# Kernel tuning notes

Measured on AMD Instinct MI355X. Metric: run time of the kernel, lower is better.

The kernel has to match this reference:

```python
import jax, jax.numpy as jnp
import numpy as np

B, V, K, D, E, NE = 32, 512, 16, 128, 32, 8192


def setup_inputs() -> dict:
    key = jax.random.key(0)
    ks = jax.random.split(key, 12)
    s = 0.05
    return {
        "vertex_features": jax.random.normal(ks[0], (B, V, D), jnp.float32),
        "atom_adj": jax.random.randint(ks[1], (B * V * K,), 0, B * V),
        "bond_adj": jax.random.randint(ks[2], (B * V * K,), 0, B * NE),
        "h0": jax.random.normal(ks[3], (B, V, D), jnp.float32),
        "lamda": jnp.full((1,), 0.5, jnp.float32),
        "alpha": jnp.full((1,), 0.1, jnp.float32),
        "l": 1,
        "edge_initial": jax.random.normal(ks[4], (B, NE, E), jnp.float32),
        "vertex_mask": jnp.ones((B, V), jnp.float32),
        "nbs_mask": jax.random.uniform(ks[5], (B, V, K), jnp.float32),
        # label_U1: (D+E) -> D ; label_U2: 2D -> D ; feature_updating: D -> D (variant=False)
        "W1": jax.random.normal(ks[6], (D, D + E), jnp.float32) * s,
        "b1": jax.random.normal(ks[7], (D,), jnp.float32) * s,
        "W2": jax.random.normal(ks[8], (D, 2 * D), jnp.float32) * s,
        "b2": jax.random.normal(ks[9], (D,), jnp.float32) * s,
        "W3": jax.random.normal(ks[10], (D, D), jnp.float32) * s,
        "b3": jax.random.normal(ks[11], (D,), jnp.float32) * s,
    }


def reference(vertex_features, atom_adj, bond_adj, h0, lamda, alpha, l,
              edge_initial, vertex_mask, nbs_mask, W1, b1, W2, b2, W3, b3):
    b, v = vertex_mask.shape
    k = nbs_mask.shape[2]
    d = vertex_features.shape[-1]
    e = edge_initial.shape[-1]
    # gather neighbor vertex and edge features (flat index, torch.index_select semantics)
    vn = vertex_features.reshape(-1, d)[atom_adj].reshape(b, v, k, d)
    en = edge_initial.reshape(-1, e)[bond_adj].reshape(b, v, k, e)
    l_neighbor = jnp.concatenate([vn, en], axis=-1)            # [b,v,k,d+e]
    nl = jax.nn.gelu(l_neighbor @ W1.T + b1, approximate=False)  # exact GELU like torch F.gelu
    nl = jnp.sum(nl * nbs_mask[..., None], axis=-2)            # masked sum over neighbors -> [b,v,d]
    hi = jnp.concatenate([nl, vertex_features], axis=-1) @ W2.T + b2
    theta = jnp.log(lamda / l + 1.0)                           # broadcast scalar (shape [1])
    support = (1.0 - alpha) * hi + alpha * h0                  # variant=False: r == support
    out = theta * (support @ W3.T + b3) + (1.0 - theta) * support
    out = out + vertex_features                                # residual=True
    return out
```

## Files before the change

kernel.cpp:

```cpp
#include <hip/hip_runtime.h>
#include <hip/hip_bf16.h>
#include <math.h>

#define NLSTR 136
#define ASTR  168

typedef __bf16 bf16x8 __attribute__((ext_vector_type(8)));
typedef float f32x4 __attribute__((ext_vector_type(4)));
typedef float f32x16 __attribute__((ext_vector_type(16)));
typedef unsigned short ushort8v __attribute__((ext_vector_type(8)));

union FragU { ushort8v u; bf16x8 b; };

static __device__ inline unsigned short f2bf(float f){
  unsigned u = __float_as_uint(f);
  u += 0x7fffu + ((u >> 16) & 1u);
  return (unsigned short)(u >> 16);
}
static __device__ inline float bf2f(unsigned short u){
  return __uint_as_float(((unsigned)u) << 16);
}
static __device__ inline unsigned pk2(float a, float b){
  union { __hip_bfloat162 h; unsigned u; } r;
  r.h = __float22bfloat162_rn(float2{a, b});
  return r.u;
}
static __device__ inline ushort8v pkcvt8(float4 a, float4 b){
  union { unsigned u[4]; ushort8v v; } r;
  r.u[0] = pk2(a.x, a.y); r.u[1] = pk2(a.z, a.w);
  r.u[2] = pk2(b.x, b.y); r.u[3] = pk2(b.z, b.w);
  return r.v;
}

static __device__ inline float gelu_f(float x){
  float u = x * x;
  float p = fmaf(u, -0.1029434273f, -2.3022084765f);
  float e = __builtin_amdgcn_exp2f(x * p);
  return x * __builtin_amdgcn_rcpf(1.0f + e);
}

#define WG_BARRIER() asm volatile("s_waitcnt lgkmcnt(0)\n\ts_barrier" ::: "memory")

__global__ __launch_bounds__(256) void prep_kernel(
    const float* __restrict__ vf, const float* __restrict__ W1,
    const float* __restrict__ W2, const float* __restrict__ W3,
    unsigned short* __restrict__ vfbf, unsigned short* __restrict__ w1f,
    unsigned short* __restrict__ w2f, unsigned short* __restrict__ w3f)
{
  int t = blockIdx.x * 256 + threadIdx.x;
  if (t < 262144){
    const float4* src = (const float4*)vf;
    float4 x = src[t * 2], y = src[t * 2 + 1];
    *(ushort8v*)(vfbf + t * 8) = pkcvt8(x, y);
    return;
  }
  int t2 = t - 262144;
  const float* s;
  unsigned short* d;
  if (t2 < 2560){
    int fragid = t2 >> 6, lane = t2 & 63;
    int nc2 = fragid / 10, kc = fragid % 10, n = lane & 31, h = lane >> 5;
    s = W1 + (nc2 * 32 + n) * 160 + kc * 16 + h * 8;
    d = w1f + t2 * 8;
  } else if (t2 < 6656){
    int t3 = t2 - 2560;
    int fragid = t3 >> 6, lane = t3 & 63;
    int kc = fragid >> 3, nc = fragid & 7, col = lane & 15, quad = lane >> 4;
    s = W2 + (nc * 16 + col) * 256 + kc * 32 + quad * 8;
    d = w2f + t3 * 8;
  } else if (t2 < 8704){
    int t3 = t2 - 6656;
    int fragid = t3 >> 6, lane = t3 & 63;
    int kc = fragid >> 3, nc = fragid & 7, col = lane & 15, quad = lane >> 4;
    s = W3 + (nc * 16 + col) * 128 + kc * 32 + quad * 8;
    d = w3f + t3 * 8;
  } else return;
#pragma unroll
  for (int j = 0; j < 8; j++) d[j] = f2bf(s[j]);
}

__global__ __launch_bounds__(256, 4) void fused_kernel(
    const unsigned short* __restrict__ vfbf,
    const float* __restrict__ vf,
    const int* __restrict__ aadj, const int* __restrict__ badj,
    const float* __restrict__ edge, const float* __restrict__ nbs,
    const float* __restrict__ h0,
    const unsigned short* __restrict__ w1f, const unsigned short* __restrict__ w2f,
    const unsigned short* __restrict__ w3f,
    const float* __restrict__ b1, const float* __restrict__ b2, const float* __restrict__ b3,
    const float* __restrict__ lamda, const float* __restrict__ alpha,
    const int* __restrict__ lval,
    float* __restrict__ out)
{
  __shared__ __align__(16) unsigned short abuf[2][32 * ASTR];
  __shared__ __align__(16) unsigned short nl_lds[16 * NLSTR];
  __shared__ __align__(16) unsigned short sup_lds[16 * NLSTR];
  __shared__ __align__(16) float nbs_lds[256];
  const int wid  = threadIdx.x >> 6;
  const int lane = threadIdx.x & 63;
  const int n32  = lane & 31;
  const int h    = lane >> 5;
  const int col  = lane & 15;
  const int quad = lane >> 4;
  const int v0   = blockIdx.x * 16;

  const int srow = threadIdx.x >> 3;
  const int ssub = threadIdx.x & 7;

  nbs_lds[threadIdx.x] = nbs[v0 * 16 + threadIdx.x];

  int a_all[8], e_all[8];
  {
    const int base = (v0 + (srow >> 4)) * 16 + (srow & 15);
#pragma unroll
    for (int p = 0; p < 8; p++){
      a_all[p] = aadj[base + 32 * p];
      e_all[p] = badj[base + 32 * p];
    }
  }

  ushort8v sv[3][2]; float4 se[3];
#pragma unroll
  for (int s = 0; s < 3; s++){
    const ushort8v* vs = (const ushort8v*)(vfbf + (size_t)a_all[s] * 128 + ssub * 16);
    sv[s][0] = vs[0]; sv[s][1] = vs[1];
    se[s] = *(const float4*)(edge + (size_t)e_all[s] * 32 + ssub * 4);
  }

  FragU bw[10];
#pragma unroll
  for (int kc = 0; kc < 10; kc++)
    bw[kc].u = *(const ushort8v*)(w1f + ((wid * 10 + kc) * 64 + lane) * 8);

  const float bb1 = b1[wid * 32 + n32];

  {
    unsigned short* dst = abuf[0] + srow * ASTR + ssub * 16;
    *(ushort8v*)dst = sv[0][0]; *(ushort8v*)(dst + 8) = sv[0][1];
    unsigned* ed = (unsigned*)(abuf[0] + srow * ASTR + 128 + ssub * 4);
    ed[0] = pk2(se[0].x, se[0].y); ed[1] = pk2(se[0].z, se[0].w);
  }

  const float4* nbsl = (const float4*)nbs_lds;

#pragma unroll
  for (int p = 0; p < 8; ++p){
    WG_BARRIER();

    if (p < 7){
      const int s = (p + 1) % 3;
      unsigned short* dst = abuf[(p + 1) & 1] + srow * ASTR + ssub * 16;
      *(ushort8v*)dst = sv[s][0]; *(ushort8v*)(dst + 8) = sv[s][1];
      unsigned* ed = (unsigned*)(abuf[(p + 1) & 1] + srow * ASTR + 128 + ssub * 4);
      ed[0] = pk2(se[s].x, se[s].y); ed[1] = pk2(se[s].z, se[s].w);
    }
    if (p < 5){
      const int s = (p + 3) % 3;
      const ushort8v* vs = (const ushort8v*)(vfbf + (size_t)a_all[p + 3] * 128 + ssub * 16);
      sv[s][0] = vs[0]; sv[s][1] = vs[1];
      se[s] = *(const float4*)(edge + (size_t)e_all[p + 3] * 32 + ssub * 4);
    }

    const float4 mAlo = nbsl[8 * p + h],     mAhi = nbsl[8 * p + 2 + h];
    const float4 mBlo = nbsl[8 * p + 4 + h], mBhi = nbsl[8 * p + 6 + h];

    const unsigned short* ab = abuf[p & 1] + n32 * ASTR + h * 8;
    f32x16 acc = {};
#pragma unroll
    for (int kc = 0; kc < 10; kc++){
      FragU fa;
      fa.u = *(const ushort8v*)(ab + kc * 16);
      acc = __builtin_amdgcn_mfma_f32_32x32x16_bf16(fa.b, bw[kc].b, acc, 0, 0, 0);
    }

    {
      float sA = gelu_f(acc[0] + bb1) * mAlo.x + gelu_f(acc[1] + bb1) * mAlo.y
               + gelu_f(acc[2] + bb1) * mAlo.z + gelu_f(acc[3] + bb1) * mAlo.w
               + gelu_f(acc[4] + bb1) * mAhi.x + gelu_f(acc[5] + bb1) * mAhi.y
               + gelu_f(acc[6] + bb1) * mAhi.z + gelu_f(acc[7] + bb1) * mAhi.w;
      float sB = gelu_f(acc[8] + bb1) * mBlo.x + gelu_f(acc[9] + bb1) * mBlo.y
               + gelu_f(acc[10] + bb1) * mBlo.z + gelu_f(acc[11] + bb1) * mBlo.w
               + gelu_f(acc[12] + bb1) * mBhi.x + gelu_f(acc[13] + bb1) * mBhi.y
               + gelu_f(acc[14] + bb1) * mBhi.z + gelu_f(acc[15] + bb1) * mBhi.w;
      sA += __shfl_xor(sA, 32, 64);
      sB += __shfl_xor(sB, 32, 64);
      if (h == 0) nl_lds[(2 * p)     * NLSTR + wid * 32 + n32] = f2bf(sA);
      else        nl_lds[(2 * p + 1) * NLSTR + wid * 32 + n32] = f2bf(sB);
    }
  }
  __syncthreads();

  const int nc0 = 2 * wid;
  const float th = logf(lamda[0] / (float)lval[0] + 1.0f);
  const float al = alpha[0];

  float h0v[2][4];
#pragma unroll
  for (int pq = 0; pq < 2; pq++){
    const int d = (nc0 + pq) * 16 + col;
#pragma unroll
    for (int r = 0; r < 4; r++)
      h0v[pq][r] = h0[(v0 + quad * 4 + r) * 128 + d];
  }

  f32x4 acc2[2] = {};
#pragma unroll
  for (int kc = 0; kc < 8; kc++){
    FragU a;
    if (kc < 4) a.u = *(const ushort8v*)(nl_lds + col * NLSTR + kc * 32 + quad * 8);
    else        a.u = *(const ushort8v*)(vfbf + (size_t)(v0 + col) * 128 + (kc - 4) * 32 + quad * 8);
#pragma unroll
    for (int pq = 0; pq < 2; pq++){
      FragU bf_;
      bf_.u = *(const ushort8v*)(w2f + ((kc * 8 + nc0 + pq) * 64 + lane) * 8);
      acc2[pq] = __builtin_amdgcn_mfma_f32_16x16x32_bf16(a.b, bf_.b, acc2[pq], 0, 0, 0);
    }
  }

  float sup[2][4];
#pragma unroll
  for (int pq = 0; pq < 2; pq++){
    const int d = (nc0 + pq) * 16 + col;
    const float bb = b2[d];
#pragma unroll
    for (int r = 0; r < 4; r++){
      float hi = acc2[pq][r] + bb;
      float s = (1.f - al) * hi + al * h0v[pq][r];
      sup[pq][r] = s;
      sup_lds[(quad * 4 + r) * NLSTR + d] = f2bf(s);
    }
  }
  __syncthreads();

  float rv[2][4];
#pragma unroll
  for (int pq = 0; pq < 2; pq++){
    const int d = (nc0 + pq) * 16 + col;
#pragma unroll
    for (int r = 0; r < 4; r++)
      rv[pq][r] = vf[(size_t)(v0 + quad * 4 + r) * 128 + d];
  }

  f32x4 acc3[2] = {};
#pragma unroll
  for (int kc = 0; kc < 4; kc++){
    FragU a;
    a.u = *(const ushort8v*)(sup_lds + col * NLSTR + kc * 32 + quad * 8);
#pragma unroll
    for (int pq = 0; pq < 2; pq++){
      FragU bf_;
      bf_.u = *(const ushort8v*)(w3f + ((kc * 8 + nc0 + pq) * 64 + lane) * 8);
      acc3[pq] = __builtin_amdgcn_mfma_f32_16x16x32_bf16(a.b, bf_.b, acc3[pq], 0, 0, 0);
    }
  }

#pragma unroll
  for (int pq = 0; pq < 2; pq++){
    const int d = (nc0 + pq) * 16 + col;
    const float bb = b3[d];
#pragma unroll
    for (int r = 0; r < 4; r++){
      const int vtx = v0 + quad * 4 + r;
      out[vtx * 128 + d] = th * (acc3[pq][r] + bb) + (1.f - th) * sup[pq][r] + rv[pq][r];
    }
  }
}

extern "C" void kernel_launch(void* const* d_in, const int* in_sizes, int n_in,
                              void* d_out, int out_size, void* d_ws, size_t ws_size,
                              hipStream_t stream)
{
  const float* vfp  = (const float*)d_in[0];
  const int*   aadj = (const int*)d_in[1];
  const int*   badj = (const int*)d_in[2];
  const float* h0   = (const float*)d_in[3];
  const float* lam  = (const float*)d_in[4];
  const float* alp  = (const float*)d_in[5];
  const int*   lv   = (const int*)d_in[6];
  const float* edge = (const float*)d_in[7];
  const float* nbs  = (const float*)d_in[9];
  const float* W1   = (const float*)d_in[10];
  const float* b1   = (const float*)d_in[11];
  const float* W2   = (const float*)d_in[12];
  const float* b2   = (const float*)d_in[13];
  const float* W3   = (const float*)d_in[14];
  const float* b3   = (const float*)d_in[15];
  float* out = (float*)d_out;

  unsigned short* w1f  = (unsigned short*)d_ws;
  unsigned short* w2f  = w1f + 20480;
  unsigned short* w3f  = w2f + 32768;
  unsigned short* vfbf = w3f + 16384;

  prep_kernel<<<1058, 256, 0, stream>>>(vfp, W1, W2, W3, vfbf, w1f, w2f, w3f);
  fused_kernel<<<1024, 256, 0, stream>>>(vfbf, vfp, aadj, badj, edge, nbs, h0,
                                         w1f, w2f, w3f, b1, b2, b3, lam, alp, lv, out);
}
```

Baseline: 137.0 us.

## Gather neighbor rows straight into MFMA A-fragments, removing LDS staging and barriers

The per-neighbor-batch A operand no longer goes through a double-buffered LDS tile with workgroup barriers. Each lane loads its own vertex and edge slices from global memory into registers laid out as MFMA fragments, and the next batch's loads are interleaved with the current MFMAs. Bias is folded into the accumulator init, nbs mask values are read directly from global memory, s_setprio is raised around the MFMA chain, and the occupancy hint in launch_bounds is dropped. The cost is redundant global loads: all four waves gather the same 32 rows. Register pressure also rises, which may lower occupancy.

```diff
diff --git a/kernel.cpp b/kernel.cpp
--- a/kernel.cpp
+++ b/kernel.cpp
@@ -3,7 +3,6 @@
 #include <math.h>
 
 #define NLSTR 136
-#define ASTR  168
 
 typedef __bf16 bf16x8 __attribute__((ext_vector_type(8)));
 typedef float f32x4 __attribute__((ext_vector_type(4)));
@@ -38,8 +37,6 @@
   float e = __builtin_amdgcn_exp2f(x * p);
   return x * __builtin_amdgcn_rcpf(1.0f + e);
 }
-
-#define WG_BARRIER() asm volatile("s_waitcnt lgkmcnt(0)\n\ts_barrier" ::: "memory")
 
 __global__ __launch_bounds__(256) void prep_kernel(
     const float* __restrict__ vf, const float* __restrict__ W1,
@@ -79,7 +76,7 @@
   for (int j = 0; j < 8; j++) d[j] = f2bf(s[j]);
 }
 
-__global__ __launch_bounds__(256, 4) void fused_kernel(
+__global__ __launch_bounds__(256) void fused_kernel(
     const unsigned short* __restrict__ vfbf,
     const float* __restrict__ vf,
     const int* __restrict__ aadj, const int* __restrict__ badj,
@@ -92,10 +89,8 @@
     const int* __restrict__ lval,
     float* __restrict__ out)
 {
-  __shared__ __align__(16) unsigned short abuf[2][32 * ASTR];
   __shared__ __align__(16) unsigned short nl_lds[16 * NLSTR];
   __shared__ __align__(16) unsigned short sup_lds[16 * NLSTR];
-  __shared__ __align__(16) float nbs_lds[256];
   const int wid  = threadIdx.x >> 6;
   const int lane = threadIdx.x & 63;
   const int n32  = lane & 31;
@@ -104,27 +99,14 @@
   const int quad = lane >> 4;
   const int v0   = blockIdx.x * 16;
 
-  const int srow = threadIdx.x >> 3;
-  const int ssub = threadIdx.x & 7;
-
-  nbs_lds[threadIdx.x] = nbs[v0 * 16 + threadIdx.x];
-
-  int a_all[8], e_all[8];
+  int a_idx[8], e_idx[8];
   {
-    const int base = (v0 + (srow >> 4)) * 16 + (srow & 15);
+    const int base = v0 * 16 + n32;
 #pragma unroll
     for (int p = 0; p < 8; p++){
-      a_all[p] = aadj[base + 32 * p];
-      e_all[p] = badj[base + 32 * p];
-    }
-  }
-
-  ushort8v sv[3][2]; float4 se[3];
-#pragma unroll
-  for (int s = 0; s < 3; s++){
-    const ushort8v* vs = (const ushort8v*)(vfbf + (size_t)a_all[s] * 128 + ssub * 16);
-    sv[s][0] = vs[0]; sv[s][1] = vs[1];
-    se[s] = *(const float4*)(edge + (size_t)e_all[s] * 32 + ssub * 4);
+      a_idx[p] = aadj[base + 32 * p];
+      e_idx[p] = badj[base + 32 * p];
+    }
   }
 
   FragU bw[10];
@@ -133,55 +115,64 @@
     bw[kc].u = *(const ushort8v*)(w1f + ((wid * 10 + kc) * 64 + lane) * 8);
 
   const float bb1 = b1[wid * 32 + n32];
-
+  const float4* nbs4 = (const float4*)nbs;
+
+  FragU va[8]; float4 ef[4];
   {
-    unsigned short* dst = abuf[0] + srow * ASTR + ssub * 16;
-    *(ushort8v*)dst = sv[0][0]; *(ushort8v*)(dst + 8) = sv[0][1];
-    unsigned* ed = (unsigned*)(abuf[0] + srow * ASTR + 128 + ssub * 4);
-    ed[0] = pk2(se[0].x, se[0].y); ed[1] = pk2(se[0].z, se[0].w);
-  }
-
-  const float4* nbsl = (const float4*)nbs_lds;
+    const ushort8v* vs = (const ushort8v*)(vfbf + (size_t)a_idx[0] * 128 + h * 8);
+#pragma unroll
+    for (int kc = 0; kc < 8; kc++) va[kc].u = vs[2 * kc];
+    const float4* es = (const float4*)(edge + (size_t)e_idx[0] * 32 + h * 8);
+    ef[0] = es[0]; ef[1] = es[1]; ef[2] = es[4]; ef[3] = es[5];
+  }
 
 #pragma unroll
   for (int p = 0; p < 8; ++p){
-    WG_BARRIER();
-
-    if (p < 7){
-      const int s = (p + 1) % 3;
-      unsigned short* dst = abuf[(p + 1) & 1] + srow * ASTR + ssub * 16;
-      *(ushort8v*)dst = sv[s][0]; *(ushort8v*)(dst + 8) = sv[s][1];
-      unsigned* ed = (unsigned*)(abuf[(p + 1) & 1] + srow * ASTR + 128 + ssub * 4);
-      ed[0] = pk2(se[s].x, se[s].y); ed[1] = pk2(se[s].z, se[s].w);
-    }
-    if (p < 5){
-      const int s = (p + 3) % 3;
-      const ushort8v* vs = (const ushort8v*)(vfbf + (size_t)a_all[p + 3] * 128 + ssub * 16);
-      sv[s][0] = vs[0]; sv[s][1] = vs[1];
-      se[s] = *(const float4*)(edge + (size_t)e_all[p + 3] * 32 + ssub * 4);
-    }
-
-    const float4 mAlo = nbsl[8 * p + h],     mAhi = nbsl[8 * p + 2 + h];
-    const float4 mBlo = nbsl[8 * p + 4 + h], mBhi = nbsl[8 * p + 6 + h];
-
-    const unsigned short* ab = abuf[p & 1] + n32 * ASTR + h * 8;
-    f32x16 acc = {};
-#pragma unroll
-    for (int kc = 0; kc < 10; kc++){
-      FragU fa;
-      fa.u = *(const ushort8v*)(ab + kc * 16);
-      acc = __builtin_amdgcn_mfma_f32_32x32x16_bf16(fa.b, bw[kc].b, acc, 0, 0, 0);
-    }
-
+    const int pn = (p < 7) ? p + 1 : 7;
+
+    FragU ea0, ea1;
     {
-      float sA = gelu_f(acc[0] + bb1) * mAlo.x + gelu_f(acc[1] + bb1) * mAlo.y
-               + gelu_f(acc[2] + bb1) * mAlo.z + gelu_f(acc[3] + bb1) * mAlo.w
-               + gelu_f(acc[4] + bb1) * mAhi.x + gelu_f(acc[5] + bb1) * mAhi.y
-               + gelu_f(acc[6] + bb1) * mAhi.z + gelu_f(acc[7] + bb1) * mAhi.w;
-      float sB = gelu_f(acc[8] + bb1) * mBlo.x + gelu_f(acc[9] + bb1) * mBlo.y
-               + gelu_f(acc[10] + bb1) * mBlo.z + gelu_f(acc[11] + bb1) * mBlo.w
-               + gelu_f(acc[12] + bb1) * mBhi.x + gelu_f(acc[13] + bb1) * mBhi.y
-               + gelu_f(acc[14] + bb1) * mBhi.z + gelu_f(acc[15] + bb1) * mBhi.w;
+      union { unsigned u[4]; ushort8v v; } r0, r1;
+      r0.u[0] = pk2(ef[0].x, ef[0].y); r0.u[1] = pk2(ef[0].z, ef[0].w);
+      r0.u[2] = pk2(ef[1].x, ef[1].y); r0.u[3] = pk2(ef[1].z, ef[1].w);
+      r1.u[0] = pk2(ef[2].x, ef[2].y); r1.u[1] = pk2(ef[2].z, ef[2].w);
+      r1.u[2] = pk2(ef[3].x, ef[3].y); r1.u[3] = pk2(ef[3].z, ef[3].w);
+      ea0.u = r0.v; ea1.u = r1.v;
+    }
+    {
+      const float4* es = (const float4*)(edge + (size_t)e_idx[pn] * 32 + h * 8);
+      ef[0] = es[0]; ef[1] = es[1]; ef[2] = es[4]; ef[3] = es[5];
+    }
+    const ushort8v* vs = (const ushort8v*)(vfbf + (size_t)a_idx[pn] * 128 + h * 8);
+
+    f32x16 acc;
+#pragma unroll
+    for (int j = 0; j < 16; j++) acc[j] = bb1;
+    __builtin_amdgcn_s_setprio(1);
+    acc = __builtin_amdgcn_mfma_f32_32x32x16_bf16(va[0].b, bw[0].b, acc, 0, 0, 0); va[0].u = vs[0];
+    acc = __builtin_amdgcn_mfma_f32_32x32x16_bf16(va[1].b, bw[1].b, acc, 0, 0, 0); va[1].u = vs[2];
+    acc = __builtin_amdgcn_mfma_f32_32x32x16_bf16(va[2].b, bw[2].b, acc, 0, 0, 0); va[2].u = vs[4];
+    acc = __builtin_amdgcn_mfma_f32_32x32x16_bf16(va[3].b, bw[3].b, acc, 0, 0, 0); va[3].u = vs[6];
+    acc = __builtin_amdgcn_mfma_f32_32x32x16_bf16(va[4].b, bw[4].b, acc, 0, 0, 0); va[4].u = vs[8];
+    acc = __builtin_amdgcn_mfma_f32_32x32x16_bf16(va[5].b, bw[5].b, acc, 0, 0, 0); va[5].u = vs[10];
+    acc = __builtin_amdgcn_mfma_f32_32x32x16_bf16(va[6].b, bw[6].b, acc, 0, 0, 0); va[6].u = vs[12];
+    acc = __builtin_amdgcn_mfma_f32_32x32x16_bf16(va[7].b, bw[7].b, acc, 0, 0, 0); va[7].u = vs[14];
+    acc = __builtin_amdgcn_mfma_f32_32x32x16_bf16(ea0.b,  bw[8].b, acc, 0, 0, 0);
+    acc = __builtin_amdgcn_mfma_f32_32x32x16_bf16(ea1.b,  bw[9].b, acc, 0, 0, 0);
+    __builtin_amdgcn_s_setprio(0);
+
+    {
+      const int vA = v0 + 2 * p;
+      const float4 mAlo = nbs4[vA * 4 + h],       mAhi = nbs4[vA * 4 + 2 + h];
+      const float4 mBlo = nbs4[(vA + 1) * 4 + h], mBhi = nbs4[(vA + 1) * 4 + 2 + h];
+      float sA = fmaf(gelu_f(acc[0]),  mAlo.x, gelu_f(acc[1])  * mAlo.y)
+               + fmaf(gelu_f(acc[2]),  mAlo.z, gelu_f(acc[3])  * mAlo.w)
+               + fmaf(gelu_f(acc[4]),  mAhi.x, gelu_f(acc[5])  * mAhi.y)
+               + fmaf(gelu_f(acc[6]),  mAhi.z, gelu_f(acc[7])  * mAhi.w);
+      float sB = fmaf(gelu_f(acc[8]),  mBlo.x, gelu_f(acc[9])  * mBlo.y)
+               + fmaf(gelu_f(acc[10]), mBlo.z, gelu_f(acc[11]) * mBlo.w)
+               + fmaf(gelu_f(acc[12]), mBhi.x, gelu_f(acc[13]) * mBhi.y)
+               + fmaf(gelu_f(acc[14]), mBhi.z, gelu_f(acc[15]) * mBhi.w);
       sA += __shfl_xor(sA, 32, 64);
       sB += __shfl_xor(sB, 32, 64);
       if (h == 0) nl_lds[(2 * p)     * NLSTR + wid * 32 + n32] = f2bf(sA);
```

New measurement: 168.9 us. 23.3% more time.
